# Kernel optimization log

Measured on AMD Instinct MI355X. Metric: run time of the kernel, lower is better.

## Reference

```python
import jax, jax.numpy as jnp
import numpy as np

N = 10000   # nodes
E = 80000   # edges per graph (avg degree 8)
H = 32      # hidden width (hard-coded in module)
VD0 = 2048  # visual_dim for gcn_0
VD1 = 256   # visual_dim // 8 for gcn_b21


def setup_inputs() -> dict:
    key = jax.random.key(0)
    ks = jax.random.split(key, 16)
    rn = lambda k, s, sc=1.0: jax.random.normal(k, s, dtype=jnp.float32) * sc
    return {
        "x": rn(ks[0], (N, 9)),
        "vis0": rn(ks[1], (N, VD0)),
        "vis1": rn(ks[2], (N, VD1)),
        "edge_index0": jax.random.randint(ks[3], (2, E), 0, N),
        "edge_index1": jax.random.randint(ks[4], (2, E), 0, N),
        # input_mlp: Linear(9,32) -> BatchNorm1d(32) (eval) -> PReLU -> Dropout(0) -> Linear(32,32)
        "W_in1": rn(ks[5], (9, H), 0.3), "b_in1": jnp.zeros((H,), jnp.float32),
        "bn_gamma": jnp.ones((H,), jnp.float32), "bn_beta": jnp.zeros((H,), jnp.float32),
        "bn_mean": jnp.zeros((H,), jnp.float32), "bn_var": jnp.ones((H,), jnp.float32),
        "prelu_a": jnp.asarray(0.25, jnp.float32),
        "W_in2": rn(ks[6], (H, H), 0.15), "b_in2": jnp.zeros((H,), jnp.float32),
        "w_node": rn(ks[7], (H, 1), 0.15), "b_node": jnp.zeros((1,), jnp.float32),
        "W_c0": rn(ks[8], (H, H), 0.15), "b_c0": jnp.zeros((H,), jnp.float32),
        "W_c1": rn(ks[9], (H, H), 0.15), "b_c1": jnp.zeros((H,), jnp.float32),
        "w_p0": rn(ks[10], (H, 1), 0.15), "b_p0": jnp.zeros((1,), jnp.float32),
        "w_p1": rn(ks[11], (H, 1), 0.15), "b_p1": jnp.zeros((1,), jnp.float32),
    }


def _cm_cos_conv(h, edge_index, vis, W, b):
    # gather-weight-scatter: w_e = cos(vis[src], vis[dst]); out_i = (sum_e->i w_e * h[src_e]) @ W + b
    src, dst = edge_index[0], edge_index[1]
    vn = vis * jax.lax.rsqrt(jnp.sum(vis * vis, axis=-1, keepdims=True) + 1e-8)
    w = jnp.sum(vn[src] * vn[dst], axis=-1)  # [E] cosine similarity per edge
    agg = jax.ops.segment_sum(h[src] * w[:, None], dst, num_segments=h.shape[0])  # [N,H]
    return agg @ W + b  # conv_activation=None -> identity


def reference(x, vis0, vis1, edge_index0, edge_index1, W_in1, b_in1, bn_gamma, bn_beta, bn_mean, bn_var, prelu_a, W_in2, b_in2, w_node, b_node, W_c0, b_c0, W_c1, b_c1, w_p0, b_p0, w_p1, b_p1):
    h = x @ W_in1 + b_in1
    h = bn_gamma * (h - bn_mean) * jax.lax.rsqrt(bn_var + 1e-5) + bn_beta
    h = jnp.where(h >= 0, h, prelu_a * h)  # PReLU (single shared slope)
    h = h @ W_in2 + b_in2                   # [N,32] shared for graphs 0 and 4
    nodes_scores = (h @ w_node + b_node)[:, 0]
    h0 = _cm_cos_conv(h, edge_index0, vis0, W_c0, b_c0)
    h1 = _cm_cos_conv(h, edge_index1, vis1, W_c1, b_c1)
    s0 = (h0 @ w_p0 + b_p0)[:, 0]
    s1 = (h1 @ w_p1 + b_p1)[:, 0]
    return nodes_scores + s0 + s1
```

## Files before the change

### kernel.cpp

```cpp
#include <hip/hip_runtime.h>

#define N_NODES 10000
#define NE      80000
#define H       32
#define VD0     2048
#define VD1     256

#define NODE_BLOCKS  40
#define NC_BLOCKS    2500
#define HIST_BLOCKS  313
#define PREP_BLOCKS  (NODE_BLOCKS + 2 * NC_BLOCKS + HIST_BLOCKS)

#define EDGE0_PHASES  4
#define EDGE0_GBLK    2500
#define EDGE0_BLOCKS  (EDGE0_PHASES * EDGE0_GBLK)
#define EDGE1_BLOCKS  2500
#define EDGE_BLOCKS   (EDGE0_BLOCKS + EDGE1_BLOCKS)

__device__ inline unsigned short f2bf_rne(float f) {
    unsigned int u = __float_as_uint(f);
    u += 0x7fffu + ((u >> 16) & 1u);
    return (unsigned short)(u >> 16);
}
__device__ inline float bflo(unsigned int u) { return __uint_as_float(u << 16); }
__device__ inline float bfhi(unsigned int u) { return __uint_as_float(u & 0xffff0000u); }

__device__ inline float dot8_bf16(uint4 a, uint4 b) {
    float s;
    s  = bflo(a.x) * bflo(b.x) + bfhi(a.x) * bfhi(b.x);
    s += bflo(a.y) * bflo(b.y) + bfhi(a.y) * bfhi(b.y);
    s += bflo(a.z) * bflo(b.z) + bfhi(a.z) * bfhi(b.z);
    s += bflo(a.w) * bflo(b.w) + bfhi(a.w) * bfhi(b.w);
    return s;
}
__device__ inline float dot4_bf16(uint2 a, uint2 b) {
    return bflo(a.x) * bflo(b.x) + bfhi(a.x) * bfhi(b.x)
         + bflo(a.y) * bflo(b.y) + bfhi(a.y) * bfhi(b.y);
}

template <int VD>
__device__ inline void normconv_node(const float* __restrict__ vis,
                                     unsigned short* __restrict__ vn,
                                     int node, int lane)
{
    const float4* v = (const float4*)(vis + (size_t)node * VD);
    float4 f[VD / 256];
    float acc = 0.f;
    #pragma unroll
    for (int it = 0; it < VD / 256; it++) {
        f[it] = v[it * 64 + lane];
        acc += f[it].x * f[it].x + f[it].y * f[it].y + f[it].z * f[it].z + f[it].w * f[it].w;
    }
    #pragma unroll
    for (int o = 32; o; o >>= 1) acc += __shfl_xor(acc, o);
    const float inv = rsqrtf(acc + 1e-8f);
    ushort4* o4 = (ushort4*)(vn + (size_t)node * VD);
    #pragma unroll
    for (int it = 0; it < VD / 256; it++) {
        ushort4 r;
        r.x = f2bf_rne(f[it].x * inv);
        r.y = f2bf_rne(f[it].y * inv);
        r.z = f2bf_rne(f[it].z * inv);
        r.w = f2bf_rne(f[it].w * inv);
        o4[it * 64 + lane] = r;
    }
}

__global__ __launch_bounds__(256) void prep_kernel(
    const float* __restrict__ x,
    const float* __restrict__ vis0, const float* __restrict__ vis1,
    const int* __restrict__ ei0, const int* __restrict__ ei1,
    const float* __restrict__ W_in1, const float* __restrict__ b_in1,
    const float* __restrict__ bn_gamma, const float* __restrict__ bn_beta,
    const float* __restrict__ bn_mean, const float* __restrict__ bn_var,
    const float* __restrict__ prelu_a,
    const float* __restrict__ W_in2, const float* __restrict__ b_in2,
    const float* __restrict__ w_node, const float* __restrict__ b_node,
    const float* __restrict__ W_c0, const float* __restrict__ b_c0,
    const float* __restrict__ W_c1, const float* __restrict__ b_c1,
    const float* __restrict__ w_p0, const float* __restrict__ b_p0,
    const float* __restrict__ w_p1, const float* __restrict__ b_p1,
    float* __restrict__ out, float* __restrict__ p0w, float* __restrict__ p1w,
    unsigned short* __restrict__ vn0, unsigned short* __restrict__ vn1,
    int* __restrict__ deg0, int* __restrict__ deg1)
{
    const int bid = blockIdx.x;
    const int t   = threadIdx.x;

    if (bid < NODE_BLOCKS) {
        __shared__ float sW1[9 * H];
        __shared__ float sW2[H * H];
        __shared__ float sU0[H], sU1[H], sWn[H];
        __shared__ float sB1[H], sB2[H], sSc[H], sSh[H];
        __shared__ float sC;

        for (int i = t; i < 9 * H; i += 256) sW1[i] = W_in1[i];
        for (int i = t; i < H * H; i += 256) sW2[i] = W_in2[i];
        if (t < H) {
            sB1[t] = b_in1[t];
            sB2[t] = b_in2[t];
            float sc = bn_gamma[t] * rsqrtf(bn_var[t] + 1e-5f);
            sSc[t] = sc;
            sSh[t] = bn_beta[t] - bn_mean[t] * sc;
            sWn[t] = w_node[t];
            float u0 = 0.f, u1 = 0.f;
            for (int j = 0; j < H; j++) {
                u0 += W_c0[t * H + j] * w_p0[j];
                u1 += W_c1[t * H + j] * w_p1[j];
            }
            sU0[t] = u0; sU1[t] = u1;
        }
        if (t == 0) {
            float c0 = b_p0[0], c1 = b_p1[0];
            for (int j = 0; j < H; j++) { c0 += b_c0[j] * w_p0[j]; c1 += b_c1[j] * w_p1[j]; }
            sC = c0 + c1 + b_node[0];
        }
        __syncthreads();

        const float a = prelu_a[0];
        const int n = bid * 256 + t;
        if (n >= N_NODES) return;

        float xi[9];
        #pragma unroll
        for (int i = 0; i < 9; i++) xi[i] = x[n * 9 + i];

        float tt[H];
        #pragma unroll
        for (int j = 0; j < H; j++) {
            float s = sB1[j];
            #pragma unroll
            for (int i = 0; i < 9; i++) s += xi[i] * sW1[i * H + j];
            s = s * sSc[j] + sSh[j];
            tt[j] = s >= 0.f ? s : a * s;
        }

        float ns = 0.f, p0 = 0.f, p1 = 0.f;
        #pragma unroll
        for (int k = 0; k < H; k++) {
            float h = sB2[k];
            #pragma unroll
            for (int j = 0; j < H; j++) h += tt[j] * sW2[j * H + k];
            ns += h * sWn[k];
            p0 += h * sU0[k];
            p1 += h * sU1[k];
        }
        out[n] = ns + sC;
        p0w[n] = p0;
        p1w[n] = p1;
    } else if (bid < NODE_BLOCKS + NC_BLOCKS) {
        const int node = ((bid - NODE_BLOCKS) * 256 + t) >> 6;
        if (node < N_NODES) normconv_node<VD0>(vis0, vn0, node, t & 63);
    } else if (bid < NODE_BLOCKS + 2 * NC_BLOCKS) {
        const int node = ((bid - NODE_BLOCKS - NC_BLOCKS) * 256 + t) >> 6;
        if (node < N_NODES) normconv_node<VD1>(vis1, vn1, node, t & 63);
    } else {
        const int e = (bid - NODE_BLOCKS - 2 * NC_BLOCKS) * 256 + t;
        if (e < NE) {
            atomicAdd(&deg0[ei0[NE + e]], 1);
            atomicAdd(&deg1[ei1[NE + e]], 1);
        }
    }
}

__global__ __launch_bounds__(1024) void scan_kernel(
    const int* __restrict__ deg0, int* __restrict__ row0, int* __restrict__ cur0,
    const int* __restrict__ deg1, int* __restrict__ row1, int* __restrict__ cur1)
{
    const int* deg = blockIdx.x ? deg1 : deg0;
    int* row_start = blockIdx.x ? row1 : row0;
    int* cursor    = blockIdx.x ? cur1 : cur0;

    __shared__ int s[1024];
    const int t = threadIdx.x;
    const int base = t * 10;
    int local[10];
    int sum = 0;
    #pragma unroll
    for (int k = 0; k < 10; k++) {
        int v = (base + k < N_NODES) ? deg[base + k] : 0;
        local[k] = v;
        sum += v;
    }
    s[t] = sum;
    __syncthreads();
    for (int off = 1; off < 1024; off <<= 1) {
        int v = 0;
        if (t >= off) v = s[t - off];
        __syncthreads();
        if (t >= off) s[t] += v;
        __syncthreads();
    }
    int excl = s[t] - sum;
    #pragma unroll
    for (int k = 0; k < 10; k++) {
        if (base + k < N_NODES) {
            row_start[base + k] = excl;
            cursor[base + k] = excl;
            excl += local[k];
        }
    }
    if (t == 1023) row_start[N_NODES] = s[1023];
}

__global__ __launch_bounds__(256) void scatter_kernel(
    const int* __restrict__ ei0, int* __restrict__ cur0, int* __restrict__ csr0,
    const int* __restrict__ ei1, int* __restrict__ cur1, int* __restrict__ csr1)
{
    const int e = blockIdx.x * 256 + threadIdx.x;
    if (e < NE) {
        int d = ei0[NE + e];
        csr0[atomicAdd(&cur0[d], 1)] = ei0[e];
        d = ei1[NE + e];
        csr1[atomicAdd(&cur1[d], 1)] = ei1[e];
    }
}

__global__ __launch_bounds__(256) void edge_kernel_fused(
    const unsigned short* __restrict__ vn0,
    const int* __restrict__ row0, const int* __restrict__ csr0,
    const float* __restrict__ p0w,
    const unsigned short* __restrict__ vn1,
    const int* __restrict__ row1, const int* __restrict__ csr1,
    const float* __restrict__ p1w,
    float* __restrict__ out)
{
    const int bid  = blockIdx.x;
    const int lane = threadIdx.x & 63;

    if (bid < EDGE0_BLOCKS) {
        const int phase = bid / EDGE0_GBLK;
        const int group = bid % EDGE0_GBLK;
        const int d     = group * 4 + (threadIdx.x >> 6);
        const int koff  = phase * 512;
        const int beg = row0[d];
        const int end = row0[d + 1];
        if (beg == end) return;

        const uint4 dreg = ((const uint4*)(vn0 + (size_t)d * VD0 + koff))[lane];
        float partial = 0.f;
        int j = beg;
        for (; j + 3 < end; j += 4) {
            const int s0 = csr0[j], s1 = csr0[j + 1], s2 = csr0[j + 2], s3 = csr0[j + 3];
            const uint4 r0 = ((const uint4*)(vn0 + (size_t)s0 * VD0 + koff))[lane];
            const uint4 r1 = ((const uint4*)(vn0 + (size_t)s1 * VD0 + koff))[lane];
            const uint4 r2 = ((const uint4*)(vn0 + (size_t)s2 * VD0 + koff))[lane];
            const uint4 r3 = ((const uint4*)(vn0 + (size_t)s3 * VD0 + koff))[lane];
            partial += dot8_bf16(dreg, r0) * p0w[s0];
            partial += dot8_bf16(dreg, r1) * p0w[s1];
            partial += dot8_bf16(dreg, r2) * p0w[s2];
            partial += dot8_bf16(dreg, r3) * p0w[s3];
        }
        for (; j < end; j++) {
            const int s0 = csr0[j];
            const uint4 r0 = ((const uint4*)(vn0 + (size_t)s0 * VD0 + koff))[lane];
            partial += dot8_bf16(dreg, r0) * p0w[s0];
        }
        #pragma unroll
        for (int o = 32; o; o >>= 1) partial += __shfl_down(partial, o);
        if (lane == 0) atomicAdd(&out[d], partial);
    } else {
        const int d = (bid - EDGE0_BLOCKS) * 4 + (threadIdx.x >> 6);
        const int beg = row1[d];
        const int end = row1[d + 1];
        if (beg == end) return;
        const uint2 dreg = ((const uint2*)(vn1 + (size_t)d * VD1))[lane];
        float partial = 0.f;
        int j = beg;
        for (; j + 3 < end; j += 4) {
            const int s0 = csr1[j], s1 = csr1[j + 1], s2 = csr1[j + 2], s3 = csr1[j + 3];
            const uint2 r0 = ((const uint2*)(vn1 + (size_t)s0 * VD1))[lane];
            const uint2 r1 = ((const uint2*)(vn1 + (size_t)s1 * VD1))[lane];
            const uint2 r2 = ((const uint2*)(vn1 + (size_t)s2 * VD1))[lane];
            const uint2 r3 = ((const uint2*)(vn1 + (size_t)s3 * VD1))[lane];
            partial += dot4_bf16(dreg, r0) * p1w[s0];
            partial += dot4_bf16(dreg, r1) * p1w[s1];
            partial += dot4_bf16(dreg, r2) * p1w[s2];
            partial += dot4_bf16(dreg, r3) * p1w[s3];
        }
        for (; j < end; j++) {
            const int s0 = csr1[j];
            const uint2 r0 = ((const uint2*)(vn1 + (size_t)s0 * VD1))[lane];
            partial += dot4_bf16(dreg, r0) * p1w[s0];
        }
        #pragma unroll
        for (int o = 32; o; o >>= 1) partial += __shfl_down(partial, o);
        if (lane == 0) atomicAdd(&out[d], partial);
    }
}

template <int VD>
__global__ __launch_bounds__(256) void norm_kernel(const float* __restrict__ vis,
                                                   float* __restrict__ inv)
{
    const int wave = (blockIdx.x * 256 + threadIdx.x) >> 6;
    const int lane = threadIdx.x & 63;
    if (wave >= N_NODES) return;
    const float4* v = (const float4*)(vis + (size_t)wave * VD);
    float acc = 0.f;
    #pragma unroll
    for (int it = 0; it < VD / 256; it++) {
        float4 f = v[lane + it * 64];
        acc += f.x * f.x + f.y * f.y + f.z * f.z + f.w * f.w;
    }
    #pragma unroll
    for (int o = 32; o; o >>= 1) acc += __shfl_down(acc, o);
    if (lane == 0) inv[wave] = rsqrtf(acc + 1e-8f);
}

template <int VD>
__global__ __launch_bounds__(256) void edge_kernel(
    const float* __restrict__ vis, const int* __restrict__ ei,
    const float* __restrict__ inv, const float* __restrict__ p,
    float* __restrict__ out)
{
    const int wave = (blockIdx.x * 256 + threadIdx.x) >> 6;
    const int lane = threadIdx.x & 63;
    if (wave >= NE) return;
    const int src = ei[wave];
    const int dst = ei[NE + wave];
    const float4* va = (const float4*)(vis + (size_t)src * VD);
    const float4* vb = (const float4*)(vis + (size_t)dst * VD);
    float acc = 0.f;
    #pragma unroll
    for (int it = 0; it < VD / 256; it++) {
        float4 fa = va[lane + it * 64];
        float4 fb = vb[lane + it * 64];
        acc += fa.x * fb.x + fa.y * fb.y + fa.z * fb.z + fa.w * fb.w;
    }
    #pragma unroll
    for (int o = 32; o; o >>= 1) acc += __shfl_down(acc, o);
    if (lane == 0) {
        float w = acc * inv[src] * inv[dst];
        atomicAdd(&out[dst], w * p[src]);
    }
}

__global__ __launch_bounds__(256) void node_kernel_fb(
    const float* __restrict__ x,
    const float* __restrict__ W_in1, const float* __restrict__ b_in1,
    const float* __restrict__ bn_gamma, const float* __restrict__ bn_beta,
    const float* __restrict__ bn_mean, const float* __restrict__ bn_var,
    const float* __restrict__ prelu_a,
    const float* __restrict__ W_in2, const float* __restrict__ b_in2,
    const float* __restrict__ w_node, const float* __restrict__ b_node,
    const float* __restrict__ W_c0, const float* __restrict__ b_c0,
    const float* __restrict__ W_c1, const float* __restrict__ b_c1,
    const float* __restrict__ w_p0, const float* __restrict__ b_p0,
    const float* __restrict__ w_p1, const float* __restrict__ b_p1,
    float* __restrict__ out, float* __restrict__ p0w, float* __restrict__ p1w)
{
    __shared__ float sW1[9 * H];
    __shared__ float sW2[H * H];
    __shared__ float sU0[H], sU1[H], sWn[H];
    __shared__ float sB1[H], sB2[H], sSc[H], sSh[H];
    __shared__ float sC;

    const int t = threadIdx.x;
    for (int i = t; i < 9 * H; i += 256) sW1[i] = W_in1[i];
    for (int i = t; i < H * H; i += 256) sW2[i] = W_in2[i];
    if (t < H) {
        sB1[t] = b_in1[t];
        sB2[t] = b_in2[t];
        float sc = bn_gamma[t] * rsqrtf(bn_var[t] + 1e-5f);
        sSc[t] = sc;
        sSh[t] = bn_beta[t] - bn_mean[t] * sc;
        sWn[t] = w_node[t];
        float u0 = 0.f, u1 = 0.f;
        for (int j = 0; j < H; j++) {
            u0 += W_c0[t * H + j] * w_p0[j];
            u1 += W_c1[t * H + j] * w_p1[j];
        }
        sU0[t] = u0; sU1[t] = u1;
    }
    if (t == 0) {
        float c0 = b_p0[0], c1 = b_p1[0];
        for (int j = 0; j < H; j++) { c0 += b_c0[j] * w_p0[j]; c1 += b_c1[j] * w_p1[j]; }
        sC = c0 + c1 + b_node[0];
    }
    __syncthreads();

    const float a = prelu_a[0];
    const int n = blockIdx.x * 256 + t;
    if (n >= N_NODES) return;

    float xi[9];
    #pragma unroll
    for (int i = 0; i < 9; i++) xi[i] = x[n * 9 + i];

    float tt[H];
    #pragma unroll
    for (int j = 0; j < H; j++) {
        float s = sB1[j];
        #pragma unroll
        for (int i = 0; i < 9; i++) s += xi[i] * sW1[i * H + j];
        s = s * sSc[j] + sSh[j];
        tt[j] = s >= 0.f ? s : a * s;
    }

    float ns = 0.f, p0 = 0.f, p1 = 0.f;
    #pragma unroll
    for (int k = 0; k < H; k++) {
        float h = sB2[k];
        #pragma unroll
        for (int j = 0; j < H; j++) h += tt[j] * sW2[j * H + k];
        ns += h * sWn[k];
        p0 += h * sU0[k];
        p1 += h * sU1[k];
    }
    out[n] = ns + sC;
    p0w[n] = p0;
    p1w[n] = p1;
}

extern "C" void kernel_launch(void* const* d_in, const int* in_sizes, int n_in,
                              void* d_out, int out_size, void* d_ws, size_t ws_size,
                              hipStream_t stream)
{
    const float* x        = (const float*)d_in[0];
    const float* vis0     = (const float*)d_in[1];
    const float* vis1     = (const float*)d_in[2];
    const int*   ei0      = (const int*)d_in[3];
    const int*   ei1      = (const int*)d_in[4];
    const float* W_in1    = (const float*)d_in[5];
    const float* b_in1    = (const float*)d_in[6];
    const float* bn_gamma = (const float*)d_in[7];
    const float* bn_beta  = (const float*)d_in[8];
    const float* bn_mean  = (const float*)d_in[9];
    const float* bn_var   = (const float*)d_in[10];
    const float* prelu_a  = (const float*)d_in[11];
    const float* W_in2    = (const float*)d_in[12];
    const float* b_in2    = (const float*)d_in[13];
    const float* w_node   = (const float*)d_in[14];
    const float* b_node   = (const float*)d_in[15];
    const float* W_c0     = (const float*)d_in[16];
    const float* b_c0     = (const float*)d_in[17];
    const float* W_c1     = (const float*)d_in[18];
    const float* b_c1     = (const float*)d_in[19];
    const float* w_p0     = (const float*)d_in[20];
    const float* b_p0     = (const float*)d_in[21];
    const float* w_p1     = (const float*)d_in[22];
    const float* b_p1     = (const float*)d_in[23];

    float* out = (float*)d_out;

    char* ws = (char*)d_ws;
    float* p0w  = (float*)ws;                  ws += N_NODES * 4;
    float* p1w  = (float*)ws;                  ws += N_NODES * 4;
    float* inv0 = (float*)ws;                  ws += N_NODES * 4;
    float* inv1 = (float*)ws;                  ws += N_NODES * 4;
    int* deg0       = (int*)ws;                ws += N_NODES * 4;
    int* deg1       = (int*)ws;                ws += N_NODES * 4;
    int* row0       = (int*)ws;                ws += (N_NODES + 1) * 4;
    int* row1       = (int*)ws;                ws += (N_NODES + 1) * 4;
    int* cur0       = (int*)ws;                ws += N_NODES * 4;
    int* cur1       = (int*)ws;                ws += N_NODES * 4;
    int* csr0       = (int*)ws;                ws += NE * 4;
    int* csr1       = (int*)ws;                ws += NE * 4;
    unsigned short* vn0 = (unsigned short*)ws; ws += (size_t)N_NODES * VD0 * 2;
    unsigned short* vn1 = (unsigned short*)ws; ws += (size_t)N_NODES * VD1 * 2;
    const size_t need = (size_t)(ws - (char*)d_ws);

    if (ws_size >= need) {
        hipMemsetAsync(deg0, 0, 2 * N_NODES * sizeof(int), stream);

        prep_kernel<<<PREP_BLOCKS, 256, 0, stream>>>(
            x, vis0, vis1, ei0, ei1,
            W_in1, b_in1, bn_gamma, bn_beta, bn_mean, bn_var, prelu_a,
            W_in2, b_in2, w_node, b_node, W_c0, b_c0, W_c1, b_c1,
            w_p0, b_p0, w_p1, b_p1,
            out, p0w, p1w, vn0, vn1, deg0, deg1);

        scan_kernel<<<2, 1024, 0, stream>>>(deg0, row0, cur0, deg1, row1, cur1);

        scatter_kernel<<<(NE + 255) / 256, 256, 0, stream>>>(
            ei0, cur0, csr0, ei1, cur1, csr1);

        edge_kernel_fused<<<EDGE_BLOCKS, 256, 0, stream>>>(
            vn0, row0, csr0, p0w, vn1, row1, csr1, p1w, out);
    } else {
        node_kernel_fb<<<(N_NODES + 255) / 256, 256, 0, stream>>>(
            x, W_in1, b_in1, bn_gamma, bn_beta, bn_mean, bn_var, prelu_a,
            W_in2, b_in2, w_node, b_node, W_c0, b_c0, W_c1, b_c1,
            w_p0, b_p0, w_p1, b_p1, out, p0w, p1w);
        norm_kernel<VD0><<<(N_NODES * 64 + 255) / 256, 256, 0, stream>>>(vis0, inv0);
        norm_kernel<VD1><<<(N_NODES * 64 + 255) / 256, 256, 0, stream>>>(vis1, inv1);
        edge_kernel<VD0><<<(NE * 64 + 255) / 256, 256, 0, stream>>>(vis0, ei0, inv0, p0w, out);
        edge_kernel<VD1><<<(NE * 64 + 255) / 256, 256, 0, stream>>>(vis1, ei1, inv1, p1w, out);
    }
}
```

Measured before the change: 257.8 us.

## Replace CSR build with fixed-capacity per-node edge buckets and overflow fallback

Drops the degree histogram and scan kernels and instead scatters each edge into a fixed 32-slot bucket per destination node, storing the source row's byte offset and its precomputed projection weight together. Edges beyond capacity are handled inline in the scatter kernel with a serial dot product and an atomic add. The edge kernel reads counts from the cursor array, loads 8 bucket entries at a time with clamped indices and masked weights, and so no longer gathers p0w/p1w separately. This removes one kernel launch and the serial scan, at the cost of a larger workspace and a slow path for high-degree nodes.

```diff
diff --git a/kernel.cpp b/kernel.cpp
--- a/kernel.cpp
+++ b/kernel.cpp
@@ -6,10 +6,11 @@
 #define VD0     2048
 #define VD1     256
 
+#define EDGE_CAP 32
+
 #define NODE_BLOCKS  40
 #define NC_BLOCKS    2500
-#define HIST_BLOCKS  313
-#define PREP_BLOCKS  (NODE_BLOCKS + 2 * NC_BLOCKS + HIST_BLOCKS)
+#define PREP_BLOCKS  (NODE_BLOCKS + 2 * NC_BLOCKS)
 
 #define EDGE0_PHASES  4
 #define EDGE0_GBLK    2500
@@ -24,6 +25,7 @@
 }
 __device__ inline float bflo(unsigned int u) { return __uint_as_float(u << 16); }
 __device__ inline float bfhi(unsigned int u) { return __uint_as_float(u & 0xffff0000u); }
+__device__ inline float bfs(unsigned short u) { return __uint_as_float((unsigned int)u << 16); }
 
 __device__ inline float dot8_bf16(uint4 a, uint4 b) {
     float s;
@@ -69,7 +71,6 @@
 __global__ __launch_bounds__(256) void prep_kernel(
     const float* __restrict__ x,
     const float* __restrict__ vis0, const float* __restrict__ vis1,
-    const int* __restrict__ ei0, const int* __restrict__ ei1,
     const float* __restrict__ W_in1, const float* __restrict__ b_in1,
     const float* __restrict__ bn_gamma, const float* __restrict__ bn_beta,
     const float* __restrict__ bn_mean, const float* __restrict__ bn_var,
@@ -81,8 +82,7 @@
     const float* __restrict__ w_p0, const float* __restrict__ b_p0,
     const float* __restrict__ w_p1, const float* __restrict__ b_p1,
     float* __restrict__ out, float* __restrict__ p0w, float* __restrict__ p1w,
-    unsigned short* __restrict__ vn0, unsigned short* __restrict__ vn1,
-    int* __restrict__ deg0, int* __restrict__ deg1)
+    unsigned short* __restrict__ vn0, unsigned short* __restrict__ vn1)
 {
     const int bid = blockIdx.x;
     const int t   = threadIdx.x;
@@ -151,78 +151,58 @@
     } else if (bid < NODE_BLOCKS + NC_BLOCKS) {
         const int node = ((bid - NODE_BLOCKS) * 256 + t) >> 6;
         if (node < N_NODES) normconv_node<VD0>(vis0, vn0, node, t & 63);
-    } else if (bid < NODE_BLOCKS + 2 * NC_BLOCKS) {
+    } else {
         const int node = ((bid - NODE_BLOCKS - NC_BLOCKS) * 256 + t) >> 6;
         if (node < N_NODES) normconv_node<VD1>(vis1, vn1, node, t & 63);
-    } else {
-        const int e = (bid - NODE_BLOCKS - 2 * NC_BLOCKS) * 256 + t;
-        if (e < NE) {
-            atomicAdd(&deg0[ei0[NE + e]], 1);
-            atomicAdd(&deg1[ei1[NE + e]], 1);
-        }
-    }
-}
-
-__global__ __launch_bounds__(1024) void scan_kernel(
-    const int* __restrict__ deg0, int* __restrict__ row0, int* __restrict__ cur0,
-    const int* __restrict__ deg1, int* __restrict__ row1, int* __restrict__ cur1)
-{
-    const int* deg = blockIdx.x ? deg1 : deg0;
-    int* row_start = blockIdx.x ? row1 : row0;
-    int* cursor    = blockIdx.x ? cur1 : cur0;
-
-    __shared__ int s[1024];
-    const int t = threadIdx.x;
-    const int base = t * 10;
-    int local[10];
-    int sum = 0;
-    #pragma unroll
-    for (int k = 0; k < 10; k++) {
-        int v = (base + k < N_NODES) ? deg[base + k] : 0;
-        local[k] = v;
-        sum += v;
-    }
-    s[t] = sum;
-    __syncthreads();
-    for (int off = 1; off < 1024; off <<= 1) {
-        int v = 0;
-        if (t >= off) v = s[t - off];
-        __syncthreads();
-        if (t >= off) s[t] += v;
-        __syncthreads();
-    }
-    int excl = s[t] - sum;
-    #pragma unroll
-    for (int k = 0; k < 10; k++) {
-        if (base + k < N_NODES) {
-            row_start[base + k] = excl;
-            cursor[base + k] = excl;
-            excl += local[k];
-        }
-    }
-    if (t == 1023) row_start[N_NODES] = s[1023];
+    }
 }
 
 __global__ __launch_bounds__(256) void scatter_kernel(
-    const int* __restrict__ ei0, int* __restrict__ cur0, int* __restrict__ csr0,
-    const int* __restrict__ ei1, int* __restrict__ cur1, int* __restrict__ csr1)
+    const int* __restrict__ ei0, int* __restrict__ cur0, uint2* __restrict__ b0,
+    const float* __restrict__ p0w, const unsigned short* __restrict__ vn0,
+    const int* __restrict__ ei1, int* __restrict__ cur1, uint2* __restrict__ b1,
+    const float* __restrict__ p1w, const unsigned short* __restrict__ vn1,
+    float* __restrict__ out)
 {
     const int e = blockIdx.x * 256 + threadIdx.x;
-    if (e < NE) {
-        int d = ei0[NE + e];
-        csr0[atomicAdd(&cur0[d], 1)] = ei0[e];
-        d = ei1[NE + e];
-        csr1[atomicAdd(&cur1[d], 1)] = ei1[e];
+    if (e >= NE) return;
+    {
+        const int s = ei0[e];
+        const int d = ei0[NE + e];
+        const int pos = atomicAdd(&cur0[d], 1);
+        if (pos < EDGE_CAP) {
+            b0[d * EDGE_CAP + pos] = make_uint2((unsigned)(s * (VD0 * 2)),
+                                                __float_as_uint(p0w[s]));
+        } else {
+            const unsigned short* a = vn0 + (size_t)s * VD0;
+            const unsigned short* c = vn0 + (size_t)d * VD0;
+            float acc = 0.f;
+            for (int i = 0; i < VD0; i++) acc += bfs(a[i]) * bfs(c[i]);
+            atomicAdd(&out[d], acc * p0w[s]);
+        }
+    }
+    {
+        const int s = ei1[e];
+        const int d = ei1[NE + e];
+        const int pos = atomicAdd(&cur1[d], 1);
+        if (pos < EDGE_CAP) {
+            b1[d * EDGE_CAP + pos] = make_uint2((unsigned)(s * (VD1 * 2)),
+                                                __float_as_uint(p1w[s]));
+        } else {
+            const unsigned short* a = vn1 + (size_t)s * VD1;
+            const unsigned short* c = vn1 + (size_t)d * VD1;
+            float acc = 0.f;
+            for (int i = 0; i < VD1; i++) acc += bfs(a[i]) * bfs(c[i]);
+            atomicAdd(&out[d], acc * p1w[s]);
+        }
     }
 }
 
 __global__ __launch_bounds__(256) void edge_kernel_fused(
     const unsigned short* __restrict__ vn0,
-    const int* __restrict__ row0, const int* __restrict__ csr0,
-    const float* __restrict__ p0w,
+    const uint2* __restrict__ b0, const int* __restrict__ cur0,
     const unsigned short* __restrict__ vn1,
-    const int* __restrict__ row1, const int* __restrict__ csr1,
-    const float* __restrict__ p1w,
+    const uint2* __restrict__ b1, const int* __restrict__ cur1,
     float* __restrict__ out)
 {
     const int bid  = blockIdx.x;
@@ -232,56 +212,68 @@
         const int phase = bid / EDGE0_GBLK;
         const int group = bid % EDGE0_GBLK;
         const int d     = group * 4 + (threadIdx.x >> 6);
-        const int koff  = phase * 512;
-        const int beg = row0[d];
-        const int end = row0[d + 1];
-        if (beg == end) return;
-
-        const uint4 dreg = ((const uint4*)(vn0 + (size_t)d * VD0 + koff))[lane];
+        int cnt = cur0[d];
+        if (cnt <= 0) return;
+        cnt = cnt < EDGE_CAP ? cnt : EDGE_CAP;
+        const int last = cnt - 1;
+
+        const char* base = (const char*)vn0;
+        const int koffB  = phase * 1024 + lane * 16;
+        const uint4 dreg = *(const uint4*)(base + d * (VD0 * 2) + koffB);
+        const uint2* eb  = b0 + d * EDGE_CAP;
+
         float partial = 0.f;
-        int j = beg;
-        for (; j + 3 < end; j += 4) {
-            const int s0 = csr0[j], s1 = csr0[j + 1], s2 = csr0[j + 2], s3 = csr0[j + 3];
-            const uint4 r0 = ((const uint4*)(vn0 + (size_t)s0 * VD0 + koff))[lane];
-            const uint4 r1 = ((const uint4*)(vn0 + (size_t)s1 * VD0 + koff))[lane];
-            const uint4 r2 = ((const uint4*)(vn0 + (size_t)s2 * VD0 + koff))[lane];
-            const uint4 r3 = ((const uint4*)(vn0 + (size_t)s3 * VD0 + koff))[lane];
-            partial += dot8_bf16(dreg, r0) * p0w[s0];
-            partial += dot8_bf16(dreg, r1) * p0w[s1];
-            partial += dot8_bf16(dreg, r2) * p0w[s2];
-            partial += dot8_bf16(dreg, r3) * p0w[s3];
-        }
-        for (; j < end; j++) {
-            const int s0 = csr0[j];
-            const uint4 r0 = ((const uint4*)(vn0 + (size_t)s0 * VD0 + koff))[lane];
-            partial += dot8_bf16(dreg, r0) * p0w[s0];
+        for (int j = 0; j < cnt; j += 8) {
+            uint2 e[8];
+            #pragma unroll
+            for (int k = 0; k < 8; k++) {
+                int jj = j + k;
+                jj = jj > last ? last : jj;
+                e[k] = eb[jj];
+            }
+            uint4 r[8];
+            #pragma unroll
+            for (int k = 0; k < 8; k++)
+                r[k] = *(const uint4*)(base + e[k].x + koffB);
+            #pragma unroll
+            for (int k = 0; k < 8; k++) {
+                const float pw = (j + k <= last) ? __uint_as_float(e[k].y) : 0.f;
+                partial += dot8_bf16(dreg, r[k]) * pw;
+            }
         }
         #pragma unroll
         for (int o = 32; o; o >>= 1) partial += __shfl_down(partial, o);
         if (lane == 0) atomicAdd(&out[d], partial);
     } else {
         const int d = (bid - EDGE0_BLOCKS) * 4 + (threadIdx.x >> 6);
-        const int beg = row1[d];
-        const int end = row1[d + 1];
-        if (beg == end) return;
-        const uint2 dreg = ((const uint2*)(vn1 + (size_t)d * VD1))[lane];
+        int cnt = cur1[d];
+        if (cnt <= 0) return;
+        cnt = cnt < EDGE_CAP ? cnt : EDGE_CAP;
+        const int last = cnt - 1;
+
+        const char* base = (const char*)vn1;
+        const int koffB  = lane * 8;
+        const uint2 dreg = *(const uint2*)(base + d * (VD1 * 2) + koffB);
+        const uint2* eb  = b1 + d * EDGE_CAP;
+
         float partial = 0.f;
-        int j = beg;
-        for (; j + 3 < end; j += 4) {
-            const int s0 = csr1[j], s1 = csr1[j + 1], s2 = csr1[j + 2], s3 = csr1[j + 3];
-            const uint2 r0 = ((const uint2*)(vn1 + (size_t)s0 * VD1))[lane];
-            const uint2 r1 = ((const uint2*)(vn1 + (size_t)s1 * VD1))[lane];
-            const uint2 r2 = ((const uint2*)(vn1 + (size_t)s2 * VD1))[lane];
-            const uint2 r3 = ((const uint2*)(vn1 + (size_t)s3 * VD1))[lane];
-            partial += dot4_bf16(dreg, r0) * p1w[s0];
-            partial += dot4_bf16(dreg, r1) * p1w[s1];
-            partial += dot4_bf16(dreg, r2) * p1w[s2];
-            partial += dot4_bf16(dreg, r3) * p1w[s3];
-        }
-        for (; j < end; j++) {
-            const int s0 = csr1[j];
-            const uint2 r0 = ((const uint2*)(vn1 + (size_t)s0 * VD1))[lane];
-            partial += dot4_bf16(dreg, r0) * p1w[s0];
+        for (int j = 0; j < cnt; j += 8) {
+            uint2 e[8];
+            #pragma unroll
+            for (int k = 0; k < 8; k++) {
+                int jj = j + k;
+                jj = jj > last ? last : jj;
+                e[k] = eb[jj];
+            }
+            uint2 r[8];
+            #pragma unroll
+            for (int k = 0; k < 8; k++)
+                r[k] = *(const uint2*)(base + e[k].x + koffB);
+            #pragma unroll
+            for (int k = 0; k < 8; k++) {
+                const float pw = (j + k <= last) ? __uint_as_float(e[k].y) : 0.f;
+                partial += dot4_bf16(dreg, r[k]) * pw;
+            }
         }
         #pragma unroll
         for (int o = 32; o; o >>= 1) partial += __shfl_down(partial, o);
@@ -449,35 +441,30 @@
     float* p1w  = (float*)ws;                  ws += N_NODES * 4;
     float* inv0 = (float*)ws;                  ws += N_NODES * 4;
     float* inv1 = (float*)ws;                  ws += N_NODES * 4;
-    int* deg0       = (int*)ws;                ws += N_NODES * 4;
-    int* deg1       = (int*)ws;                ws += N_NODES * 4;
-    int* row0       = (int*)ws;                ws += (N_NODES + 1) * 4;
-    int* row1       = (int*)ws;                ws += (N_NODES + 1) * 4;
-    int* cur0       = (int*)ws;                ws += N_NODES * 4;
-    int* cur1       = (int*)ws;                ws += N_NODES * 4;
-    int* csr0       = (int*)ws;                ws += NE * 4;
-    int* csr1       = (int*)ws;                ws += NE * 4;
     unsigned short* vn0 = (unsigned short*)ws; ws += (size_t)N_NODES * VD0 * 2;
     unsigned short* vn1 = (unsigned short*)ws; ws += (size_t)N_NODES * VD1 * 2;
+    uint2* b0   = (uint2*)ws;                  ws += (size_t)N_NODES * EDGE_CAP * 8;
+    uint2* b1   = (uint2*)ws;                  ws += (size_t)N_NODES * EDGE_CAP * 8;
+    int* cur0   = (int*)ws;                    ws += N_NODES * 4;
+    int* cur1   = (int*)ws;                    ws += N_NODES * 4;
     const size_t need = (size_t)(ws - (char*)d_ws);
 
     if (ws_size >= need) {
-        hipMemsetAsync(deg0, 0, 2 * N_NODES * sizeof(int), stream);
+        hipMemsetAsync(cur0, 0, 2 * N_NODES * sizeof(int), stream);
 
         prep_kernel<<<PREP_BLOCKS, 256, 0, stream>>>(
-            x, vis0, vis1, ei0, ei1,
+            x, vis0, vis1,
             W_in1, b_in1, bn_gamma, bn_beta, bn_mean, bn_var, prelu_a,
             W_in2, b_in2, w_node, b_node, W_c0, b_c0, W_c1, b_c1,
             w_p0, b_p0, w_p1, b_p1,
-            out, p0w, p1w, vn0, vn1, deg0, deg1);
-
-        scan_kernel<<<2, 1024, 0, stream>>>(deg0, row0, cur0, deg1, row1, cur1);
+            out, p0w, p1w, vn0, vn1);
 
         scatter_kernel<<<(NE + 255) / 256, 256, 0, stream>>>(
-            ei0, cur0, csr0, ei1, cur1, csr1);
+            ei0, cur0, b0, p0w, vn0,
+            ei1, cur1, b1, p1w, vn1, out);
 
         edge_kernel_fused<<<EDGE_BLOCKS, 256, 0, stream>>>(
-            vn0, row0, csr0, p0w, vn1, row1, csr1, p1w, out);
+            vn0, b0, cur0, vn1, b1, cur1, out);
     } else {
         node_kernel_fb<<<(N_NODES + 255) / 256, 256, 0, stream>>>(
             x, W_in1, b_in1, bn_gamma, bn_beta, bn_mean, bn_var, prelu_a,
```

Result: faster. 238.8 us (-7.4%).
